# Optimization experiments

Measured on AMD Instinct MI355X. Metric: run time of the kernel, lower is better.

## Reference

```python
import jax, jax.numpy as jnp
import numpy as np

VOCAB, D, H = 32000, 1024, 16
DH = D // H
DFF = 4 * D
EPS = 1e-5


def layer_norm(x, g, b):
    mu = jnp.mean(x, axis=-1, keepdims=True)
    var = jnp.var(x, axis=-1, keepdims=True)
    return (x - mu) * jax.lax.rsqrt(var + EPS) * g + b


def pos_enc(seq_len, d_model):
    # faithful to the torch double-loop: angle = pos / 10000**(2*i/d) for even index i
    pos = jnp.arange(seq_len, dtype=jnp.float32)[:, None]          # [S,1]
    i_even = jnp.arange(0, d_model, 2, dtype=jnp.float32)[None, :]  # [1,D/2]
    angle = pos / jnp.power(10000.0, 2.0 * i_even / d_model)        # [S,D/2]
    pe = jnp.zeros((seq_len, d_model), dtype=jnp.float32)
    pe = pe.at[:, 0::2].set(jnp.sin(angle))
    pe = pe.at[:, 1::2].set(jnp.cos(angle))
    return pe


def setup_inputs() -> dict:
    key = jax.random.key(0)
    ks = jax.random.split(key, 16)
    s = 0.02
    return {
        "tokens": jax.random.randint(ks[0], (4, 2048), 0, VOCAB),
        "emb": jax.random.normal(ks[1], (VOCAB, D), jnp.float32) * s,
        "in_proj_w": jax.random.normal(ks[2], (3 * D, D), jnp.float32) * s,
        "in_proj_b": jnp.zeros((3 * D,), jnp.float32),
        "out_proj_w": jax.random.normal(ks[3], (D, D), jnp.float32) * s,
        "out_proj_b": jnp.zeros((D,), jnp.float32),
        "w1": jax.random.normal(ks[4], (DFF, D), jnp.float32) * s,
        "b1": jnp.zeros((DFF,), jnp.float32),
        "w2": jax.random.normal(ks[5], (D, DFF), jnp.float32) * s,
        "b2": jnp.zeros((D,), jnp.float32),
        "g1": jnp.ones((D,), jnp.float32),
        "beta1": jnp.zeros((D,), jnp.float32),
        "g2": jnp.ones((D,), jnp.float32),
        "beta2": jnp.zeros((D,), jnp.float32),
    }


def reference(tokens, emb, in_proj_w, in_proj_b, out_proj_w, out_proj_b,
              w1, b1, w2, b2, g1, beta1, g2, beta2):
    B, S = tokens.shape
    x = emb[tokens] + pos_enc(S, D)[None, :, :]                 # [B,S,D]
    # multi-head self-attention (eval mode, no dropout)
    qkv = x @ in_proj_w.T + in_proj_b                           # [B,S,3D]
    q, k, v = jnp.split(qkv, 3, axis=-1)
    q = q.reshape(B, S, H, DH)
    k = k.reshape(B, S, H, DH)
    v = v.reshape(B, S, H, DH)
    scores = jnp.einsum("bqhd,bkhd->bhqk", q, k) / jnp.sqrt(jnp.float32(DH))
    attn = jax.nn.softmax(scores, axis=-1)
    ctx = jnp.einsum("bhqk,bkhd->bqhd", attn, v).reshape(B, S, D)
    attn_out = ctx @ out_proj_w.T + out_proj_b
    h = layer_norm(x + attn_out, g1, beta1)
    ff = jax.nn.relu(h @ w1.T + b1) @ w2.T + b2
    return layer_norm(h + ff, g2, beta2)
```

## Files before the change

### kernel.cpp

```cpp
#include <hip/hip_runtime.h>
#include <math.h>

#define DMODEL 1024
#define NH 16
#define DHEAD 64
#define DFF 4096
#define BATCH 4
#define SEQ 2048
#define MROWS (BATCH * SEQ)
#define LNEPS 1e-5f
#define NT (SEQ / 64)

typedef __attribute__((ext_vector_type(8))) short bf16x8;
typedef __attribute__((ext_vector_type(4))) float f32x4;

__device__ inline unsigned short f2bf(float f) {
  unsigned int u = __float_as_uint(f);
  unsigned int r = (u + 0x7fffu + ((u >> 16) & 1u)) >> 16;
  return (unsigned short)r;
}

__device__ inline void gload16(const unsigned short* g, char* l) {
  __builtin_amdgcn_global_load_lds(
      (const __attribute__((address_space(1))) unsigned int*)g,
      (__attribute__((address_space(3))) unsigned int*)l, 16, 0, 0);
}

__device__ inline float fexp2(float x) {
  float r;
  asm("v_exp_f32 %0, %1" : "=v"(r) : "v"(x));
  return r;
}
__device__ inline unsigned int cvtpk(float lo, float hi) {
  unsigned int r;
  asm("v_cvt_pk_bf16_f32 %0, %1, %2" : "=v"(r) : "v"(lo), "v"(hi));
  return r;
}

__global__ __launch_bounds__(256)
void embed_kernel(const int* __restrict__ tokens, const float* __restrict__ emb,
                  float* __restrict__ X, unsigned short* __restrict__ Xb) {
  const int HALF = DMODEL / 2;
  int idx = blockIdx.x * 256 + threadIdx.x;
  if (idx >= MROWS * HALF) return;
  int row = idx / HALF;
  int j = idx - row * HALF;
  int s = row & (SEQ - 1);
  int tok = tokens[row];
  float2 e = ((const float2*)(emb + (size_t)tok * DMODEL))[j];
  float denom = powf(10000.0f, (2.0f * (float)(2 * j)) / (float)DMODEL);
  float ang = (float)s / denom;
  float sn, cs;
  sincosf(ang, &sn, &cs);
  float2 o;
  o.x = e.x + sn;
  o.y = e.y + cs;
  ((float2*)(X + (size_t)row * DMODEL))[j] = o;
  ushort2 ob;
  ob.x = f2bf(o.x); ob.y = f2bf(o.y);
  ((ushort2*)(Xb + (size_t)row * DMODEL))[j] = ob;
}

__global__ __launch_bounds__(256)
void cvt_kernel(const float* __restrict__ in, unsigned short* __restrict__ out, int n4) {
  int i = blockIdx.x * 256 + threadIdx.x;
  if (i >= n4) return;
  float4 v = ((const float4*)in)[i];
  ushort4 o;
  o.x = f2bf(v.x); o.y = f2bf(v.y); o.z = f2bf(v.z); o.w = f2bf(v.w);
  ((ushort4*)out)[i] = o;
}

__global__ __launch_bounds__(256)
void gemm_bf16(const unsigned short* __restrict__ A, const unsigned short* __restrict__ B,
               const float* __restrict__ bias, const float* __restrict__ resid,
               float* __restrict__ Cf, unsigned short* __restrict__ Cb,
               int M, int N, int K, int relu) {
  __shared__ __align__(16) char smem[32768];

  const int t = threadIdx.x;
  const int lane = t & 63;
  const int wv = t >> 6;
  const int wm = wv >> 1, wn = wv & 1;
  const int fr = lane & 15;
  const int fq = lane >> 4;
  const int swz = (fr >> 1) & 3;

  const int nwg = gridDim.x;
  const int orig = blockIdx.x;
  const int q8 = nwg >> 3;
  const int wgid = (orig & 7) * q8 + (orig >> 3);
  const int stid = wgid >> 6, within = wgid & 63;
  const int sm = within & 7, sn = within >> 3;
  const int Msup = M >> 10;
  const int stm = stid % Msup, stn = stid / Msup;
  const int m0 = (stm * 8 + sm) * 128;
  const int n0 = (stn * 8 + sn) * 128;

  const int rl = lane >> 2, sl = lane & 3;
  size_t gA[2], gB[2];
  int lofs[2];
#pragma unroll
  for (int p = 0; p < 2; ++p) {
    int row = wv * 32 + p * 16 + rl;
    int c = sl ^ ((row >> 1) & 3);
    gA[p] = (size_t)(m0 + row) * K + c * 8;
    gB[p] = (size_t)(n0 + row) * K + c * 8;
    lofs[p] = (wv * 32 + p * 16) * 64;
  }

  f32x4 acc[4][4];
#pragma unroll
  for (int m = 0; m < 4; ++m)
#pragma unroll
    for (int n = 0; n < 4; ++n) acc[m][n] = (f32x4){0.f, 0.f, 0.f, 0.f};

  const int nk = K / 32;

#pragma unroll
  for (int p = 0; p < 2; ++p) {
    gload16(A + gA[p], smem + lofs[p]);
    gload16(B + gB[p], smem + 8192 + lofs[p]);
  }
  __syncthreads();

  for (int kt = 0; kt < nk; ++kt) {
    const char* cur = smem + ((kt & 1) << 14);
    if (kt + 1 < nk) {
      char* nxt = smem + (((kt + 1) & 1) << 14);
      int k0 = (kt + 1) * 32;
#pragma unroll
      for (int p = 0; p < 2; ++p) {
        gload16(A + gA[p] + k0, nxt + lofs[p]);
        gload16(B + gB[p] + k0, nxt + 8192 + lofs[p]);
      }
    }
    const unsigned short* Al = (const unsigned short*)cur;
    const unsigned short* Bl = (const unsigned short*)(cur + 8192);
    bf16x8 af[4], bfv[4];
#pragma unroll
    for (int m = 0; m < 4; ++m) {
      int arow = wm * 64 + m * 16 + fr;
      af[m] = *(const bf16x8*)&Al[arow * 32 + ((fq ^ swz) * 8)];
    }
#pragma unroll
    for (int n = 0; n < 4; ++n) {
      int brow = wn * 64 + n * 16 + fr;
      bfv[n] = *(const bf16x8*)&Bl[brow * 32 + ((fq ^ swz) * 8)];
    }
#pragma unroll
    for (int m = 0; m < 4; ++m)
#pragma unroll
      for (int n = 0; n < 4; ++n)
        acc[m][n] = __builtin_amdgcn_mfma_f32_16x16x32_bf16(af[m], bfv[n], acc[m][n], 0, 0, 0);
    __syncthreads();
  }

  float* slab = (float*)(smem + wv * 4352);
#pragma unroll
  for (int m = 0; m < 4; ++m) {
#pragma unroll
    for (int n = 0; n < 4; ++n)
#pragma unroll
      for (int j = 0; j < 4; ++j)
        slab[(fq * 4 + j) * 68 + n * 16 + fr] = acc[m][n][j];
    int rg0 = m0 + wm * 64 + m * 16;
#pragma unroll
    for (int it = 0; it < 4; ++it) {
      int u = it * 64 + lane;
      int row = u >> 4, seg = u & 15;
      float4 v = *(const float4*)&slab[row * 68 + seg * 4];
      int col = n0 + wn * 64 + seg * 4;
      float4 b4 = *(const float4*)&bias[col];
      v.x += b4.x; v.y += b4.y; v.z += b4.z; v.w += b4.w;
      if (relu) {
        v.x = fmaxf(v.x, 0.f); v.y = fmaxf(v.y, 0.f);
        v.z = fmaxf(v.z, 0.f); v.w = fmaxf(v.w, 0.f);
      }
      size_t idx = (size_t)(rg0 + row) * N + col;
      if (resid) {
        float4 r4 = *(const float4*)&resid[idx];
        v.x += r4.x; v.y += r4.y; v.z += r4.z; v.w += r4.w;
      }
      if (Cf) {
        *(float4*)&Cf[idx] = v;
      } else {
        ushort4 ob;
        ob.x = f2bf(v.x); ob.y = f2bf(v.y); ob.z = f2bf(v.z); ob.w = f2bf(v.w);
        *(ushort4*)&Cb[idx] = ob;
      }
    }
  }
}

__global__ __launch_bounds__(512, 4)
void attn_kernel(const unsigned short* __restrict__ qkv, unsigned short* __restrict__ ctxb) {
  __shared__ __align__(16) unsigned short Ks[2][64][64];
  __shared__ __align__(16) unsigned short Vts[2][64][64];
  __shared__ __align__(16) unsigned short Pw[8][32][64];

  const int t = threadIdx.x;
  const int lane = t & 63;
  const int wq = t >> 6;
  const int ci = lane & 15;
  const int hi = lane >> 4;
  const int bid = blockIdx.x;
  const int bh = bid & 63;
  const int qt = bid >> 6;
  const int b = bh >> 4, h = bh & 15;
  const int q0 = qt * 256;

  const size_t RS = 3 * DMODEL;
  const unsigned short* qb = qkv + (size_t)b * SEQ * RS + h * DHEAD;
  const unsigned short* kb = qb + DMODEL;
  const unsigned short* vb = qb + 2 * DMODEL;

  bf16x8 qf[2][2];
#pragma unroll
  for (int qi = 0; qi < 2; ++qi) {
    const unsigned short* qrow = qb + (size_t)(q0 + wq * 32 + qi * 16 + ci) * RS;
#pragma unroll
    for (int s = 0; s < 2; ++s)
      qf[qi][s] = *(const bf16x8*)(qrow + s * 32 + hi * 8);
  }

  const unsigned short* kgl =
      kb + (size_t)(wq * 8 + (lane >> 3)) * RS + ((lane & 7) ^ (lane >> 3)) * 8;
  const int vrow0 = wq * 8;

  f32x4 oacc[2][4];
  float lacc[2][4];
#pragma unroll
  for (int qi = 0; qi < 2; ++qi)
#pragma unroll
    for (int n = 0; n < 4; ++n) {
      oacc[qi][n] = (f32x4){0.f, 0.f, 0.f, 0.f};
      lacc[qi][n] = 0.f;
    }

  gload16(kgl, (char*)&Ks[0][wq * 8][0]);
  {
    unsigned int vg[8];
#pragma unroll
    for (int e = 0; e < 8; ++e)
      vg[e] = vb[(size_t)(vrow0 + e) * RS + lane];
    uint4 u;
    u.x = vg[0] | (vg[1] << 16);
    u.y = vg[2] | (vg[3] << 16);
    u.z = vg[4] | (vg[5] << 16);
    u.w = vg[6] | (vg[7] << 16);
    *(uint4*)&Vts[0][lane][((wq ^ (lane & 7)) * 8)] = u;
  }
  __syncthreads();

  const float C = 0.18033688011112042f;

  for (int kt = 0; kt < NT; ++kt) {
    const int cur = kt & 1;
    const bool more = (kt + 1 < NT);
    unsigned int vg[8];
    if (more) {
      size_t off = (size_t)(kt + 1) * 64 * RS;
      gload16(kgl + off, (char*)&Ks[cur ^ 1][wq * 8][0]);
#pragma unroll
      for (int e = 0; e < 8; ++e)
        vg[e] = vb[off + (size_t)(vrow0 + e) * RS + lane];
    }

    f32x4 sacc[2][4];
#pragma unroll
    for (int qi = 0; qi < 2; ++qi)
#pragma unroll
      for (int n = 0; n < 4; ++n) sacc[qi][n] = (f32x4){0.f, 0.f, 0.f, 0.f};
#pragma unroll
    for (int s = 0; s < 2; ++s)
#pragma unroll
      for (int n = 0; n < 4; ++n) {
        int krow = n * 16 + ci;
        bf16x8 kf = *(const bf16x8*)&Ks[cur][krow][(((s * 4 + hi) ^ (krow & 7)) * 8)];
        sacc[0][n] = __builtin_amdgcn_mfma_f32_16x16x32_bf16(qf[0][s], kf, sacc[0][n], 0, 0, 0);
        sacc[1][n] = __builtin_amdgcn_mfma_f32_16x16x32_bf16(qf[1][s], kf, sacc[1][n], 0, 0, 0);
      }

#pragma unroll
    for (int qi = 0; qi < 2; ++qi)
#pragma unroll
      for (int j = 0; j < 4; ++j) {
        float p0 = fexp2(sacc[qi][0][j] * C);
        float p1 = fexp2(sacc[qi][1][j] * C);
        float p2 = fexp2(sacc[qi][2][j] * C);
        float p3 = fexp2(sacc[qi][3][j] * C);
        lacc[qi][j] += (p0 + p1) + (p2 + p3);
        unsigned int r0 = cvtpk(p0, p1);
        unsigned int r1 = cvtpk(p2, p3);
        int row = qi * 16 + hi * 4 + j;
        int r7 = row & 7;
        unsigned short* pr = &Pw[wq][row][0];
        pr[((((ci >> 3) + 0) ^ r7) * 8) + (ci & 7)] = (unsigned short)r0;
        pr[((((ci >> 3) + 2) ^ r7) * 8) + (ci & 7)] = (unsigned short)(r0 >> 16);
        pr[((((ci >> 3) + 4) ^ r7) * 8) + (ci & 7)] = (unsigned short)r1;
        pr[((((ci >> 3) + 6) ^ r7) * 8) + (ci & 7)] = (unsigned short)(r1 >> 16);
      }

#pragma unroll
    for (int s = 0; s < 2; ++s) {
      bf16x8 pf0 = *(const bf16x8*)&Pw[wq][ci][(((s * 4 + hi) ^ (ci & 7)) * 8)];
      bf16x8 pf1 = *(const bf16x8*)&Pw[wq][16 + ci][(((s * 4 + hi) ^ ((16 + ci) & 7)) * 8)];
#pragma unroll
      for (int n = 0; n < 4; ++n) {
        int drow = n * 16 + ci;
        bf16x8 vf = *(const bf16x8*)&Vts[cur][drow][(((s * 4 + hi) ^ (drow & 7)) * 8)];
        oacc[0][n] = __builtin_amdgcn_mfma_f32_16x16x32_bf16(pf0, vf, oacc[0][n], 0, 0, 0);
        oacc[1][n] = __builtin_amdgcn_mfma_f32_16x16x32_bf16(pf1, vf, oacc[1][n], 0, 0, 0);
      }
    }

    if (more) {
      uint4 u;
      u.x = vg[0] | (vg[1] << 16);
      u.y = vg[2] | (vg[3] << 16);
      u.z = vg[4] | (vg[5] << 16);
      u.w = vg[6] | (vg[7] << 16);
      *(uint4*)&Vts[cur ^ 1][lane][((wq ^ (lane & 7)) * 8)] = u;
    }
    __syncthreads();
  }

#pragma unroll
  for (int qi = 0; qi < 2; ++qi)
#pragma unroll
    for (int j = 0; j < 4; ++j) {
      float l = lacc[qi][j];
      l += __shfl_xor(l, 1);
      l += __shfl_xor(l, 2);
      l += __shfl_xor(l, 4);
      l += __shfl_xor(l, 8);
      float inv = 1.0f / l;
      int row = qi * 16 + hi * 4 + j;
      int r7 = row & 7;
      unsigned short* pr = &Pw[wq][row][0];
#pragma unroll
      for (int n = 0; n < 4; ++n)
        pr[(((2 * n + (ci >> 3)) ^ r7) * 8) + (ci & 7)] = f2bf(oacc[qi][n][j] * inv);
    }
#pragma unroll
  for (int it = 0; it < 4; ++it) {
    int u = it * 64 + lane;
    int row = u >> 3, s = u & 7;
    uint4 v = *(const uint4*)&Pw[wq][row][((s ^ (row & 7)) * 8)];
    *(uint4*)(ctxb + (size_t)(b * SEQ + q0 + wq * 32 + row) * DMODEL + h * DHEAD + s * 8) = v;
  }
}

__global__ __launch_bounds__(256)
void ln_kernel(const float* __restrict__ Z, const float* __restrict__ g,
               const float* __restrict__ bta, float* __restrict__ Y,
               unsigned short* __restrict__ Yb) {
  const int row = blockIdx.x;
  const float4* z4 = (const float4*)(Z + (size_t)row * DMODEL);
  float4 v = z4[threadIdx.x];
  float s = v.x + v.y + v.z + v.w;
  float ss = fmaf(v.x, v.x, fmaf(v.y, v.y, fmaf(v.z, v.z, v.w * v.w)));
#pragma unroll
  for (int o = 32; o >= 1; o >>= 1) {
    s += __shfl_xor(s, o);
    ss += __shfl_xor(ss, o);
  }
  __shared__ float red[8];
  int w = threadIdx.x >> 6;
  if ((threadIdx.x & 63) == 0) { red[w] = s; red[4 + w] = ss; }
  __syncthreads();
  s = red[0] + red[1] + red[2] + red[3];
  ss = red[4] + red[5] + red[6] + red[7];
  float mu = s * (1.0f / DMODEL);
  float var = ss * (1.0f / DMODEL) - mu * mu;
  float rs = rsqrtf(var + LNEPS);
  float4 gg = ((const float4*)g)[threadIdx.x];
  float4 bb = ((const float4*)bta)[threadIdx.x];
  float4 o;
  o.x = (v.x - mu) * rs * gg.x + bb.x;
  o.y = (v.y - mu) * rs * gg.y + bb.y;
  o.z = (v.z - mu) * rs * gg.z + bb.z;
  o.w = (v.w - mu) * rs * gg.w + bb.w;
  ((float4*)(Y + (size_t)row * DMODEL))[threadIdx.x] = o;
  if (Yb) {
    ushort4 ob;
    ob.x = f2bf(o.x); ob.y = f2bf(o.y); ob.z = f2bf(o.z); ob.w = f2bf(o.w);
    ((ushort4*)(Yb + (size_t)row * DMODEL))[threadIdx.x] = ob;
  }
}

extern "C" void kernel_launch(void* const* d_in, const int* in_sizes, int n_in,
                              void* d_out, int out_size, void* d_ws, size_t ws_size,
                              hipStream_t stream) {
  const int* tokens       = (const int*)d_in[0];
  const float* emb        = (const float*)d_in[1];
  const float* in_proj_w  = (const float*)d_in[2];
  const float* in_proj_b  = (const float*)d_in[3];
  const float* out_proj_w = (const float*)d_in[4];
  const float* out_proj_b = (const float*)d_in[5];
  const float* w1         = (const float*)d_in[6];
  const float* b1         = (const float*)d_in[7];
  const float* w2         = (const float*)d_in[8];
  const float* b2         = (const float*)d_in[9];
  const float* g1         = (const float*)d_in[10];
  const float* beta1      = (const float*)d_in[11];
  const float* g2         = (const float*)d_in[12];
  const float* beta2      = (const float*)d_in[13];
  float* out = (float*)d_out;

  char* ws = (char*)d_ws;
  const size_t MB = 1ull << 20;
  unsigned short* inwb  = (unsigned short*)(ws + 0 * MB);
  unsigned short* outwb = (unsigned short*)(ws + 6 * MB);
  unsigned short* w1b   = (unsigned short*)(ws + 8 * MB);
  unsigned short* w2b   = (unsigned short*)(ws + 16 * MB);
  float* x              = (float*)(ws + 24 * MB);
  unsigned short* xb    = (unsigned short*)(ws + 56 * MB);
  unsigned short* qkvb  = (unsigned short*)(ws + 72 * MB);
  unsigned short* ctxb  = (unsigned short*)(ws + 56 * MB);
  float* h              = (float*)(ws + 72 * MB);
  unsigned short* hb    = (unsigned short*)(ws + 104 * MB);
  unsigned short* ffbb  = (unsigned short*)(ws + 120 * MB);
  float* y2             = (float*)(ws + 24 * MB);

  embed_kernel<<<(MROWS * (DMODEL / 2) + 255) / 256, 256, 0, stream>>>(tokens, emb, x, xb);
  cvt_kernel<<<(3 * DMODEL * DMODEL / 4 + 255) / 256, 256, 0, stream>>>(in_proj_w, inwb, 3 * DMODEL * DMODEL / 4);
  cvt_kernel<<<(DMODEL * DMODEL / 4 + 255) / 256, 256, 0, stream>>>(out_proj_w, outwb, DMODEL * DMODEL / 4);
  cvt_kernel<<<(DFF * DMODEL / 4 + 255) / 256, 256, 0, stream>>>(w1, w1b, DFF * DMODEL / 4);
  cvt_kernel<<<(DMODEL * DFF / 4 + 255) / 256, 256, 0, stream>>>(w2, w2b, DMODEL * DFF / 4);
  gemm_bf16<<<(MROWS / 128) * (3 * DMODEL / 128), 256, 0, stream>>>(
      xb, inwb, in_proj_b, nullptr, nullptr, qkvb, MROWS, 3 * DMODEL, DMODEL, 0);
  attn_kernel<<<(SEQ / 256) * (BATCH * NH), 512, 0, stream>>>(qkvb, ctxb);
  gemm_bf16<<<(MROWS / 128) * (DMODEL / 128), 256, 0, stream>>>(
      ctxb, outwb, out_proj_b, x, h, nullptr, MROWS, DMODEL, DMODEL, 0);
  ln_kernel<<<MROWS, 256, 0, stream>>>(h, g1, beta1, h, hb);
  gemm_bf16<<<(MROWS / 128) * (DFF / 128), 256, 0, stream>>>(
      hb, w1b, b1, nullptr, nullptr, ffbb, MROWS, DFF, DMODEL, 1);
  gemm_bf16<<<(MROWS / 128) * (DMODEL / 128), 256, 0, stream>>>(
      ffbb, w2b, b2, h, y2, nullptr, MROWS, DMODEL, DFF, 0);
  ln_kernel<<<MROWS, 256, 0, stream>>>(y2, g2, beta2, out, nullptr);
}
```

Baseline: 443.3 us.

## Replace GEMM with 256x128 8-wave triple-buffered pipelined kernel; fuse weight casts

Replaces the 128x128, 4-wave, double-buffered GEMM with a 256x128 tile kernel using 8 waves, K-step 64, and a 3-stage LDS ring of 144 KB. It interleaves async global-to-LDS loads with MFMA phases using explicit vmcnt waits, barriers and setprio. The aim is to hide load latency and raise MFMA use. The four weight-conversion launches are merged into one kernel to cut launch overhead. This adds heavy LDS use, which limits occupancy, and the fixed waitcnt counts and epilogue slab reuse are fragile.

```diff
diff --git a/kernel.cpp b/kernel.cpp
--- a/kernel.cpp
+++ b/kernel.cpp
@@ -62,52 +62,111 @@
 }
 
 __global__ __launch_bounds__(256)
-void cvt_kernel(const float* __restrict__ in, unsigned short* __restrict__ out, int n4) {
+void cvt4_kernel(const float* __restrict__ a, const float* __restrict__ b,
+                 const float* __restrict__ c, const float* __restrict__ d,
+                 unsigned short* __restrict__ oa, unsigned short* __restrict__ ob,
+                 unsigned short* __restrict__ oc, unsigned short* __restrict__ od) {
   int i = blockIdx.x * 256 + threadIdx.x;
-  if (i >= n4) return;
-  float4 v = ((const float4*)in)[i];
+  const float* src; unsigned short* dst; int off;
+  if (i < 786432)       { src = a; dst = oa; off = 0; }
+  else if (i < 1048576) { src = b; dst = ob; off = 786432; }
+  else if (i < 2097152) { src = c; dst = oc; off = 1048576; }
+  else                  { src = d; dst = od; off = 2097152; }
+  int j = i - off;
+  float4 v = ((const float4*)src)[j];
   ushort4 o;
   o.x = f2bf(v.x); o.y = f2bf(v.y); o.z = f2bf(v.z); o.w = f2bf(v.w);
-  ((ushort4*)out)[i] = o;
-}
-
-__global__ __launch_bounds__(256)
-void gemm_bf16(const unsigned short* __restrict__ A, const unsigned short* __restrict__ B,
-               const float* __restrict__ bias, const float* __restrict__ resid,
-               float* __restrict__ Cf, unsigned short* __restrict__ Cb,
-               int M, int N, int K, int relu) {
-  __shared__ __align__(16) char smem[32768];
+  ((ushort4*)dst)[j] = o;
+}
+
+#define AOFF(buf) ((buf) * 49152)
+#define BOFF(buf) ((buf) * 49152 + 32768)
+
+__device__ inline void stageA(const unsigned short* Ag, char* smem, int buf,
+                              int m0, int K, int kt, int wv, int lane) {
+  int rl = lane >> 3, c = (lane & 7) ^ rl;
+#pragma unroll
+  for (int i = 0; i < 4; ++i) {
+    int r0 = (wv * 4 + i) * 8;
+    gload16(Ag + (size_t)(m0 + r0 + rl) * K + kt * 64 + c * 8,
+            smem + AOFF(buf) + r0 * 128 + lane * 16);
+  }
+}
+__device__ inline void stageB2(const unsigned short* Bg, char* smem, int buf,
+                               int n0, int K, int kt, int wv, int lane) {
+  int rl = lane >> 3, c = (lane & 7) ^ rl;
+#pragma unroll
+  for (int i = 0; i < 2; ++i) {
+    int r0 = (wv * 2 + i) * 8;
+    gload16(Bg + (size_t)(n0 + r0 + rl) * K + kt * 64 + c * 8,
+            smem + BOFF(buf) + r0 * 128 + lane * 16);
+  }
+}
+
+#define VM6 asm volatile("s_waitcnt vmcnt(6)" ::: "memory")
+#define VM0 asm volatile("s_waitcnt vmcnt(0)" ::: "memory")
+
+#define DO_PHASE(buf, mb, LOADB, STAGE_STMT, WAIT_STMT)                         \
+  {                                                                             \
+    bf16x8 af[2][2];                                                            \
+    _Pragma("unroll") for (int mm = 0; mm < 2; ++mm) {                          \
+      int arow = wm * 64 + ((mb) + mm) * 16 + fr;                               \
+      _Pragma("unroll") for (int ks = 0; ks < 2; ++ks) {                        \
+        int slot = (ks * 4 + fq) ^ (arow & 7);                                  \
+        af[mm][ks] = *(const bf16x8*)(smem + AOFF(buf) + arow * 128 + slot * 16); \
+      }                                                                         \
+    }                                                                           \
+    if (LOADB) {                                                                \
+      _Pragma("unroll") for (int n = 0; n < 4; ++n) {                           \
+        int brow = wn * 64 + n * 16 + fr;                                       \
+        _Pragma("unroll") for (int ks = 0; ks < 2; ++ks) {                      \
+          int slot = (ks * 4 + fq) ^ (brow & 7);                                \
+          bfr[n][ks] = *(const bf16x8*)(smem + BOFF(buf) + brow * 128 + slot * 16); \
+        }                                                                       \
+      }                                                                         \
+    }                                                                           \
+    STAGE_STMT;                                                                 \
+    __builtin_amdgcn_sched_barrier(0);                                          \
+    __builtin_amdgcn_s_barrier();                                               \
+    __builtin_amdgcn_sched_barrier(0);                                          \
+    __builtin_amdgcn_s_setprio(1);                                              \
+    _Pragma("unroll") for (int mm = 0; mm < 2; ++mm)                            \
+      _Pragma("unroll") for (int n = 0; n < 4; ++n)                             \
+        _Pragma("unroll") for (int ks = 0; ks < 2; ++ks)                        \
+          acc[(mb) + mm][n] = __builtin_amdgcn_mfma_f32_16x16x32_bf16(          \
+              af[mm][ks], bfr[n][ks], acc[(mb) + mm][n], 0, 0, 0);              \
+    __builtin_amdgcn_s_setprio(0);                                              \
+    WAIT_STMT;                                                                  \
+    __builtin_amdgcn_sched_barrier(0);                                          \
+    __builtin_amdgcn_s_barrier();                                               \
+    __builtin_amdgcn_sched_barrier(0);                                          \
+  }
+
+__global__ __launch_bounds__(512, 2)
+void gemm8(const unsigned short* __restrict__ A, const unsigned short* __restrict__ B,
+           const float* __restrict__ bias, const float* __restrict__ resid,
+           float* __restrict__ Cf, unsigned short* __restrict__ Cb,
+           int M, int N, int K, int relu) {
+  extern __shared__ char smem[];
 
   const int t = threadIdx.x;
   const int lane = t & 63;
   const int wv = t >> 6;
-  const int wm = wv >> 1, wn = wv & 1;
+  const int wm = wv >> 1;
+  const int wn = wv & 1;
   const int fr = lane & 15;
   const int fq = lane >> 4;
-  const int swz = (fr >> 1) & 3;
 
   const int nwg = gridDim.x;
   const int orig = blockIdx.x;
   const int q8 = nwg >> 3;
   const int wgid = (orig & 7) * q8 + (orig >> 3);
-  const int stid = wgid >> 6, within = wgid & 63;
-  const int sm = within & 7, sn = within >> 3;
+  const int stid = wgid >> 4, within = wgid & 15;
+  const int sm = within & 3, sn = within >> 2;
   const int Msup = M >> 10;
   const int stm = stid % Msup, stn = stid / Msup;
-  const int m0 = (stm * 8 + sm) * 128;
-  const int n0 = (stn * 8 + sn) * 128;
-
-  const int rl = lane >> 2, sl = lane & 3;
-  size_t gA[2], gB[2];
-  int lofs[2];
-#pragma unroll
-  for (int p = 0; p < 2; ++p) {
-    int row = wv * 32 + p * 16 + rl;
-    int c = sl ^ ((row >> 1) & 3);
-    gA[p] = (size_t)(m0 + row) * K + c * 8;
-    gB[p] = (size_t)(n0 + row) * K + c * 8;
-    lofs[p] = (wv * 32 + p * 16) * 64;
-  }
+  const int m0 = (stm * 4 + sm) * 256;
+  const int n0 = (stn * 4 + sn) * 128;
 
   f32x4 acc[4][4];
 #pragma unroll
@@ -115,45 +174,36 @@
 #pragma unroll
     for (int n = 0; n < 4; ++n) acc[m][n] = (f32x4){0.f, 0.f, 0.f, 0.f};
 
-  const int nk = K / 32;
-
-#pragma unroll
-  for (int p = 0; p < 2; ++p) {
-    gload16(A + gA[p], smem + lofs[p]);
-    gload16(B + gB[p], smem + 8192 + lofs[p]);
-  }
-  __syncthreads();
-
-  for (int kt = 0; kt < nk; ++kt) {
-    const char* cur = smem + ((kt & 1) << 14);
-    if (kt + 1 < nk) {
-      char* nxt = smem + (((kt + 1) & 1) << 14);
-      int k0 = (kt + 1) * 32;
-#pragma unroll
-      for (int p = 0; p < 2; ++p) {
-        gload16(A + gA[p] + k0, nxt + lofs[p]);
-        gload16(B + gB[p] + k0, nxt + 8192 + lofs[p]);
-      }
-    }
-    const unsigned short* Al = (const unsigned short*)cur;
-    const unsigned short* Bl = (const unsigned short*)(cur + 8192);
-    bf16x8 af[4], bfv[4];
-#pragma unroll
-    for (int m = 0; m < 4; ++m) {
-      int arow = wm * 64 + m * 16 + fr;
-      af[m] = *(const bf16x8*)&Al[arow * 32 + ((fq ^ swz) * 8)];
-    }
-#pragma unroll
-    for (int n = 0; n < 4; ++n) {
-      int brow = wn * 64 + n * 16 + fr;
-      bfv[n] = *(const bf16x8*)&Bl[brow * 32 + ((fq ^ swz) * 8)];
-    }
-#pragma unroll
-    for (int m = 0; m < 4; ++m)
-#pragma unroll
-      for (int n = 0; n < 4; ++n)
-        acc[m][n] = __builtin_amdgcn_mfma_f32_16x16x32_bf16(af[m], bfv[n], acc[m][n], 0, 0, 0);
-    __syncthreads();
+  const int nk = K / 64;
+  const int nj = nk / 2;
+
+  stageB2(B, smem, 0, n0, K, 0, wv, lane);
+  stageA (A, smem, 0, m0, K, 0, wv, lane);
+  stageB2(B, smem, 1, n0, K, 1, wv, lane);
+  stageA (A, smem, 1, m0, K, 1, wv, lane);
+  VM6;
+  __builtin_amdgcn_sched_barrier(0);
+  __builtin_amdgcn_s_barrier();
+  __builtin_amdgcn_sched_barrier(0);
+
+  for (int j = 0; j < nj - 1; ++j) {
+    const int k0 = 2 * j, k1 = 2 * j + 1;
+    const int s0k = k0 + 2, s1k = k1 + 2;
+    const int b0 = k0 % 3, b1 = k1 % 3;
+    const int sb0 = s0k % 3, sb1 = s1k % 3;
+    bf16x8 bfr[4][2];
+    DO_PHASE(b0, 0, true,  stageB2(B, smem, sb0, n0, K, s0k, wv, lane), );
+    DO_PHASE(b0, 2, false, stageA (A, smem, sb0, m0, K, s0k, wv, lane), VM6);
+    DO_PHASE(b1, 0, true,  stageB2(B, smem, sb1, n0, K, s1k, wv, lane), );
+    DO_PHASE(b1, 2, false, stageA (A, smem, sb1, m0, K, s1k, wv, lane), VM6);
+  }
+  {
+    const int b0 = (nk - 2) % 3, b1 = (nk - 1) % 3;
+    bf16x8 bfr[4][2];
+    DO_PHASE(b0, 0, true,  , );
+    DO_PHASE(b0, 2, false, , VM0);
+    DO_PHASE(b1, 0, true,  , );
+    DO_PHASE(b1, 2, false, , );
   }
 
   float* slab = (float*)(smem + wv * 4352);
@@ -424,20 +474,20 @@
   unsigned short* ffbb  = (unsigned short*)(ws + 120 * MB);
   float* y2             = (float*)(ws + 24 * MB);
 
+  const size_t GLDS = 147456;
+
   embed_kernel<<<(MROWS * (DMODEL / 2) + 255) / 256, 256, 0, stream>>>(tokens, emb, x, xb);
-  cvt_kernel<<<(3 * DMODEL * DMODEL / 4 + 255) / 256, 256, 0, stream>>>(in_proj_w, inwb, 3 * DMODEL * DMODEL / 4);
-  cvt_kernel<<<(DMODEL * DMODEL / 4 + 255) / 256, 256, 0, stream>>>(out_proj_w, outwb, DMODEL * DMODEL / 4);
-  cvt_kernel<<<(DFF * DMODEL / 4 + 255) / 256, 256, 0, stream>>>(w1, w1b, DFF * DMODEL / 4);
-  cvt_kernel<<<(DMODEL * DFF / 4 + 255) / 256, 256, 0, stream>>>(w2, w2b, DMODEL * DFF / 4);
-  gemm_bf16<<<(MROWS / 128) * (3 * DMODEL / 128), 256, 0, stream>>>(
+  cvt4_kernel<<<12288, 256, 0, stream>>>(in_proj_w, out_proj_w, w1, w2,
+                                         inwb, outwb, w1b, w2b);
+  gemm8<<<(MROWS / 256) * (3 * DMODEL / 128), 512, GLDS, stream>>>(
       xb, inwb, in_proj_b, nullptr, nullptr, qkvb, MROWS, 3 * DMODEL, DMODEL, 0);
   attn_kernel<<<(SEQ / 256) * (BATCH * NH), 512, 0, stream>>>(qkvb, ctxb);
-  gemm_bf16<<<(MROWS / 128) * (DMODEL / 128), 256, 0, stream>>>(
+  gemm8<<<(MROWS / 256) * (DMODEL / 128), 512, GLDS, stream>>>(
       ctxb, outwb, out_proj_b, x, h, nullptr, MROWS, DMODEL, DMODEL, 0);
   ln_kernel<<<MROWS, 256, 0, stream>>>(h, g1, beta1, h, hb);
-  gemm_bf16<<<(MROWS / 128) * (DFF / 128), 256, 0, stream>>>(
+  gemm8<<<(MROWS / 256) * (DFF / 128), 512, GLDS, stream>>>(
       hb, w1b, b1, nullptr, nullptr, ffbb, MROWS, DFF, DMODEL, 1);
-  gemm_bf16<<<(MROWS / 128) * (DMODEL / 128), 256, 0, stream>>>(
+  gemm8<<<(MROWS / 256) * (DMODEL / 128), 512, GLDS, stream>>>(
       ffbb, w2b, b2, h, y2, nullptr, MROWS, DMODEL, DFF, 0);
   ln_kernel<<<MROWS, 256, 0, stream>>>(y2, g2, beta2, out, nullptr);
 }
```

Result: faster. 431.8 us (-2.6%).
